# Kernel tuning notes

Hardware: AMD Instinct MI355X
Metric: run time of the kernel (lower is better)

The kernel has to match this reference:

```python
import jax, jax.numpy as jnp
import numpy as np

B, S, D = 32, 577, 768
H, Dh = 12, 64  # num_attention_heads, attention_head_size = pruned_dim // heads


def setup_inputs() -> dict:
    key = jax.random.key(0)
    ks = jax.random.split(key, 7)
    s = 1.0 / np.sqrt(D)
    return {
        "hidden_states": jax.random.normal(ks[0], (B, S, D), dtype=jnp.float32),
        "Wq": jax.random.normal(ks[1], (D, H * Dh), dtype=jnp.float32) * s,
        "bq": jnp.zeros((H * Dh,), dtype=jnp.float32),
        "Wk": jax.random.normal(ks[2], (D, H * Dh), dtype=jnp.float32) * s,
        "bk": jnp.zeros((H * Dh,), dtype=jnp.float32),
        "Wv": jax.random.normal(ks[3], (D, H * Dh), dtype=jnp.float32) * s,
        "bv": jnp.zeros((H * Dh,), dtype=jnp.float32),
    }


def reference(hidden_states, Wq, bq, Wk, bk, Wv, bv):
    def heads(x):  # [B,S,H*Dh] -> [B,H,S,Dh]
        return x.reshape(B, S, H, Dh).transpose(0, 2, 1, 3)

    q = heads(hidden_states @ Wq + bq)
    k = heads(hidden_states @ Wk + bk)
    v = heads(hidden_states @ Wv + bv)

    scale = 1.0 / np.sqrt(Dh)
    scores = jnp.einsum("bhqd,bhkd->bhqk", q, k) * scale  # [B,H,S,S]
    probs = jax.nn.softmax(scores, axis=-1)  # dropout p=0.0 -> identity
    ctx = jnp.einsum("bhqk,bhkd->bhqd", probs, v)  # [B,H,S,Dh]
    ctx = ctx.transpose(0, 2, 1, 3).reshape(B, S, H * Dh)
    return ctx
```

## Files before the change

kernel.cpp:

```cpp
#include <hip/hip_runtime.h>

#define NB 32
#define SEQ 577
#define SP 640
#define DM 768
#define NH 12
#define DH 64
#define NC 10

typedef __attribute__((ext_vector_type(8))) short bf16x8;
typedef __attribute__((ext_vector_type(4))) short bf16x4;
typedef __attribute__((ext_vector_type(4))) float f32x4;
typedef __attribute__((ext_vector_type(2))) unsigned int u32x2;
typedef __attribute__((ext_vector_type(4))) unsigned int u32x4;
typedef unsigned short u16;

__device__ __forceinline__ u16 f2bf(float f) {
  unsigned int u = __builtin_bit_cast(unsigned int, f);
  u += 0x7fffu + ((u >> 16) & 1u);
  return (u16)(u >> 16);
}

__device__ __forceinline__ unsigned int pack_bf2(float a, float b) {
  unsigned int ua = __builtin_bit_cast(unsigned int, a) + 0x8000u;
  unsigned int ub = __builtin_bit_cast(unsigned int, b) + 0x8000u;
  return __builtin_amdgcn_perm(ub, ua, 0x07060302u);
}

__device__ __forceinline__ void g2l16(const void* g, void* lds) {
  __builtin_amdgcn_global_load_lds(
      (const __attribute__((address_space(1))) void*)g,
      (__attribute__((address_space(3))) void*)lds, 16, 0, 0);
}

__global__ void cvt_x_kernel(const float* __restrict__ X, u16* __restrict__ Xb, int n4) {
  int i = blockIdx.x * 256 + threadIdx.x;
  if (i >= n4) return;
  f32x4 v = *reinterpret_cast<const f32x4*>(X + (size_t)i * 4);
  u32x2 p;
  p[0] = (unsigned)f2bf(v[0]) | ((unsigned)f2bf(v[1]) << 16);
  p[1] = (unsigned)f2bf(v[2]) | ((unsigned)f2bf(v[3]) << 16);
  *reinterpret_cast<u32x2*>(Xb + (size_t)i * 4) = p;
}

__global__ void cvt_w_kernel(const float* __restrict__ Wq, const float* __restrict__ Wk,
                             const float* __restrict__ Wv, u16* __restrict__ Wt) {
  int idx = blockIdx.x * 256 + threadIdx.x;
  int m = blockIdx.y;
  const float* W = (m == 0) ? Wq : (m == 1) ? Wk : Wv;
  int k = idx / DM, n = idx - k * DM;
  Wt[(size_t)m * DM * DM + (size_t)n * DM + k] = f2bf(W[idx]);
}

__global__ __launch_bounds__(512, 2)
void qkv_gemm_kernel(const u16* __restrict__ Xb, const u16* __restrict__ Wt,
                     const float* __restrict__ bq, const float* __restrict__ bk,
                     const float* __restrict__ bv,
                     u16* __restrict__ Qw, u16* __restrict__ Kw, u16* __restrict__ Vw) {
  __shared__ alignas(16) u16 As[2][32 * 512];
  __shared__ alignas(16) u16 Bs[2][32 * 512];

  const int tid = threadIdx.x;
  const int lane = tid & 63;
  const int wid = tid >> 6;
  const int wm = wid >> 2, wn = wid & 3;
  const int l15 = lane & 15, lq = lane >> 4;

  const int flat = (blockIdx.z * 3 + blockIdx.y) * 80 + blockIdx.x;
  const int xcd = flat & 7;
  const int j8 = flat >> 3;
  const int xi = j8 / 9;
  const int yz = j8 - xi * 9;
  const int mt = xi * 8 + xcd;
  const int nt = yz % 3;
  const int qkv = yz / 3;

  const u16* Wm = Wt + (size_t)qkv * DM * DM;
  const float* bias = (qkv == 0) ? bq : (qkv == 1) ? bk : bv;

  const u16* gA[4];
  const u16* gB[4];
#pragma unroll
  for (int s = 0; s < 4; ++s) {
    const int e = wid * 4 + s;
    const int ti = e >> 1, hh = e & 1;
    int r = mt * 256 + ti * 16 + l15;
    int br = r / SP;
    int tr = r - br * SP;
    if (tr >= SEQ) tr = SEQ - 1;
    gA[s] = Xb + (size_t)(br * SEQ + tr) * DM + hh * 32 + lq * 8;
    gB[s] = Wm + (size_t)(nt * 256 + ti * 16 + l15) * DM + hh * 32 + lq * 8;
  }

  f32x4 acc[8][4];
#pragma unroll
  for (int i = 0; i < 8; ++i)
#pragma unroll
    for (int j = 0; j < 4; ++j)
#pragma unroll
      for (int r = 0; r < 4; ++r) acc[i][j][r] = 0.0f;

  auto stageA = [&](int buf, int kt) {
#pragma unroll
    for (int s = 0; s < 4; ++s)
      g2l16(gA[s] + kt * 64, &As[buf][(wid * 4 + s) * 512]);
  };
  auto stageB = [&](int buf, int kt) {
#pragma unroll
    for (int s = 0; s < 4; ++s)
      g2l16(gB[s] + kt * 64, &Bs[buf][(wid * 4 + s) * 512]);
  };

  stageA(0, 0);
  stageB(0, 0);
  asm volatile("s_waitcnt vmcnt(0)" ::: "memory");
  __builtin_amdgcn_s_barrier();

  const int NKT = DM / 64;
  for (int kt = 0; kt < NKT; ++kt) {
    const int buf = kt & 1;
    const bool more = (kt + 1 < NKT);
    bf16x8 af[4][2], bfr[4][2];

#pragma unroll
    for (int i = 0; i < 4; ++i)
#pragma unroll
      for (int h = 0; h < 2; ++h)
        af[i][h] = *reinterpret_cast<const bf16x8*>(
            &As[buf][(((wm * 8 + i) * 2 + h) * 64 + lane) * 8]);
#pragma unroll
    for (int j = 0; j < 2; ++j)
#pragma unroll
      for (int h = 0; h < 2; ++h)
        bfr[j][h] = *reinterpret_cast<const bf16x8*>(
            &Bs[buf][(((wn * 4 + j) * 2 + h) * 64 + lane) * 8]);
    if (more) stageA(buf ^ 1, kt + 1);
    __builtin_amdgcn_s_barrier();
    __builtin_amdgcn_s_setprio(1);
#pragma unroll
    for (int i = 0; i < 4; ++i)
#pragma unroll
      for (int j = 0; j < 2; ++j)
#pragma unroll
        for (int h = 0; h < 2; ++h)
          acc[i][j] = __builtin_amdgcn_mfma_f32_16x16x32_bf16(af[i][h], bfr[j][h], acc[i][j], 0, 0, 0);
    __builtin_amdgcn_s_setprio(0);
    __builtin_amdgcn_s_barrier();

#pragma unroll
    for (int j = 2; j < 4; ++j)
#pragma unroll
      for (int h = 0; h < 2; ++h)
        bfr[j][h] = *reinterpret_cast<const bf16x8*>(
            &Bs[buf][(((wn * 4 + j) * 2 + h) * 64 + lane) * 8]);
    if (more) stageB(buf ^ 1, kt + 1);
    __builtin_amdgcn_s_barrier();
    __builtin_amdgcn_s_setprio(1);
#pragma unroll
    for (int i = 0; i < 4; ++i)
#pragma unroll
      for (int j = 2; j < 4; ++j)
#pragma unroll
        for (int h = 0; h < 2; ++h)
          acc[i][j] = __builtin_amdgcn_mfma_f32_16x16x32_bf16(af[i][h], bfr[j][h], acc[i][j], 0, 0, 0);
    __builtin_amdgcn_s_setprio(0);
    __builtin_amdgcn_s_barrier();

#pragma unroll
    for (int i = 0; i < 4; ++i)
#pragma unroll
      for (int h = 0; h < 2; ++h)
        af[i][h] = *reinterpret_cast<const bf16x8*>(
            &As[buf][(((wm * 8 + 4 + i) * 2 + h) * 64 + lane) * 8]);
    __builtin_amdgcn_s_barrier();
    __builtin_amdgcn_s_setprio(1);
#pragma unroll
    for (int i = 0; i < 4; ++i)
#pragma unroll
      for (int j = 2; j < 4; ++j)
#pragma unroll
        for (int h = 0; h < 2; ++h)
          acc[4 + i][j] = __builtin_amdgcn_mfma_f32_16x16x32_bf16(af[i][h], bfr[j][h], acc[4 + i][j], 0, 0, 0);
    __builtin_amdgcn_s_setprio(0);
    __builtin_amdgcn_s_barrier();

    __builtin_amdgcn_s_setprio(1);
#pragma unroll
    for (int i = 0; i < 4; ++i)
#pragma unroll
      for (int j = 0; j < 2; ++j)
#pragma unroll
        for (int h = 0; h < 2; ++h)
          acc[4 + i][j] = __builtin_amdgcn_mfma_f32_16x16x32_bf16(af[i][h], bfr[j][h], acc[4 + i][j], 0, 0, 0);
    __builtin_amdgcn_s_setprio(0);
    asm volatile("s_waitcnt vmcnt(0)" ::: "memory");
    __builtin_amdgcn_s_barrier();
  }

  const float sfold = 0.18033688011112042f;
#pragma unroll
  for (int j = 0; j < 4; ++j) {
    const int col = nt * 256 + wn * 64 + j * 16 + l15;
    const int h = col >> 6;
    const int d = col & 63;
    const float bb = bias[col];
#pragma unroll
    for (int i = 0; i < 8; ++i) {
      const int rg = mt * 256 + wm * 128 + i * 16 + lq * 4;
      const int br = rg / SP;
      const int tr = rg - br * SP;
      if (qkv == 2) {
        float v0 = acc[i][j][0] + bb, v1 = acc[i][j][1] + bb;
        float v2 = acc[i][j][2] + bb, v3 = acc[i][j][3] + bb;
        u32x2 p;
        p[0] = (unsigned)f2bf(v0) | ((unsigned)f2bf(v1) << 16);
        p[1] = (unsigned)f2bf(v2) | ((unsigned)f2bf(v3) << 16);
        size_t o = ((size_t)(br * NH + h) * DH + d) * SP + tr;
        *reinterpret_cast<u32x2*>(Vw + o) = p;
      } else {
        u16* dst = ((qkv == 0) ? Qw : Kw) + ((size_t)(br * NH + h) * SP + tr) * DH + d;
#pragma unroll
        for (int r = 0; r < 4; ++r) {
          float v = acc[i][j][r] + bb;
          if (qkv == 0) v *= sfold;
          dst[r * DH] = f2bf(v);
        }
      }
    }
  }
}

#if __has_builtin(__builtin_amdgcn_mfma_f32_16x16x16bf16_1k)
#define MFMA16(a, b, c) __builtin_amdgcn_mfma_f32_16x16x16bf16_1k(a, b, c, 0, 0, 0)
#define HAVE_MFMA16 1
#elif __has_builtin(__builtin_amdgcn_mfma_f32_16x16x16_bf16)
#define MFMA16(a, b, c) __builtin_amdgcn_mfma_f32_16x16x16_bf16(a, b, c, 0, 0, 0)
#define HAVE_MFMA16 1
#else
#define HAVE_MFMA16 0
#endif

__global__ __launch_bounds__(256)
void attn_kernel(const u16* __restrict__ Qw, const u16* __restrict__ Kw,
                 const u16* __restrict__ Vw, float* __restrict__ out) {
  __shared__ alignas(16) u16 Kc[2][8 * 64 * 8];
  __shared__ alignas(16) u16 Vc[2][16 * 64 * 4];

  const int tid = threadIdx.x;
  const int lane = tid & 63;
  const int wid = tid >> 6;
  const int l15 = lane & 15, lq = lane >> 4;

  const int flat = blockIdx.y * 5 + blockIdx.x;
  const int w = (flat & 7) * 240 + (flat >> 3);
  const int qx = w % 5;
  const int bh = w / 5;
  const int b = bh / NH;
  const int h = bh - b * NH;
  const int q0 = qx * 128 + wid * 32;

  const u16* Qb = Qw + (size_t)bh * SP * DH;
  const u16* Kb = Kw + (size_t)bh * SP * DH;
  const u16* Vb = Vw + (size_t)bh * DH * SP;

  bf16x8 qf[2][2];
#pragma unroll
  for (int qt = 0; qt < 2; ++qt)
#pragma unroll
    for (int hf = 0; hf < 2; ++hf)
      qf[qt][hf] = *reinterpret_cast<const bf16x8*>(
          &Qb[(q0 + qt * 16 + l15) * DH + hf * 32 + lq * 8]);

  const u16* gK = Kb + (size_t)(wid * 16 + l15) * DH + lq * 8;
  const u16* gV = Vb + (size_t)(wid * 16 + l15) * SP + lq * 4;

  float mrow[2] = {-__builtin_inff(), -__builtin_inff()};
  float lrow[2] = {0.0f, 0.0f};
  f32x4 acc[2][4];
#pragma unroll
  for (int qt = 0; qt < 2; ++qt)
#pragma unroll
    for (int dt = 0; dt < 4; ++dt)
#pragma unroll
      for (int r = 0; r < 4; ++r) acc[qt][dt][r] = 0.0f;

  g2l16(gK, &Kc[0][(wid * 2 + 0) * 512]);
  g2l16(gK + 32, &Kc[0][(wid * 2 + 1) * 512]);
  {
    u32x2 v[4];
#pragma unroll
    for (int t = 0; t < 4; ++t)
      v[t] = *reinterpret_cast<const u32x2*>(gV + t * 16);
#pragma unroll
    for (int t = 0; t < 4; ++t)
      *reinterpret_cast<u32x2*>(&Vc[0][((wid * 4 + t) * 64 + lane) * 4]) = v[t];
  }
  __syncthreads();

  for (int c = 0; c < NC; ++c) {
    const int cur = c & 1;
    const int c0 = c * 64;
    u32x2 vn[4];
    if (c + 1 < NC) {
      const u16* gKn = gK + (size_t)(c0 + 64) * DH;
      g2l16(gKn, &Kc[cur ^ 1][(wid * 2 + 0) * 512]);
      g2l16(gKn + 32, &Kc[cur ^ 1][(wid * 2 + 1) * 512]);
#pragma unroll
      for (int t = 0; t < 4; ++t)
        vn[t] = *reinterpret_cast<const u32x2*>(gV + (c0 + 64) + t * 16);
    }

    f32x4 s[2][4];
    __builtin_amdgcn_s_setprio(1);
#pragma unroll
    for (int t = 0; t < 4; ++t) {
      bf16x8 kf0 = *reinterpret_cast<const bf16x8*>(&Kc[cur][((t * 2 + 0) * 64 + lane) * 8]);
      bf16x8 kf1 = *reinterpret_cast<const bf16x8*>(&Kc[cur][((t * 2 + 1) * 64 + lane) * 8]);
#pragma unroll
      for (int qt = 0; qt < 2; ++qt) {
        f32x4 z;
#pragma unroll
        for (int r = 0; r < 4; ++r) z[r] = 0.0f;
        z = __builtin_amdgcn_mfma_f32_16x16x32_bf16(kf0, qf[qt][0], z, 0, 0, 0);
        z = __builtin_amdgcn_mfma_f32_16x16x32_bf16(kf1, qf[qt][1], z, 0, 0, 0);
        s[qt][t] = z;
      }
    }
    __builtin_amdgcn_s_setprio(0);
    if (c0 + 64 > SEQ) {
#pragma unroll
      for (int qt = 0; qt < 2; ++qt)
#pragma unroll
        for (int t = 0; t < 4; ++t)
#pragma unroll
          for (int r = 0; r < 4; ++r) {
            int key = c0 + t * 16 + lq * 4 + r;
            s[qt][t][r] = (key < SEQ) ? s[qt][t][r] : -__builtin_inff();
          }
    }
    float alpha[2];
    unsigned int pku[2][4][2];
#pragma unroll
    for (int qt = 0; qt < 2; ++qt) {
      float mx = s[qt][0][0];
#pragma unroll
      for (int t = 0; t < 4; ++t)
#pragma unroll
        for (int r = 0; r < 4; ++r) mx = fmaxf(mx, s[qt][t][r]);
      mx = fmaxf(mx, __shfl_xor(mx, 16));
      mx = fmaxf(mx, __shfl_xor(mx, 32));
      float mn = fmaxf(mrow[qt], mx);
      alpha[qt] = __builtin_amdgcn_exp2f(mrow[qt] - mn);
      mrow[qt] = mn;
      float sm = 0.0f;
#pragma unroll
      for (int t = 0; t < 4; ++t) {
        float p0 = __builtin_amdgcn_exp2f(s[qt][t][0] - mn);
        float p1 = __builtin_amdgcn_exp2f(s[qt][t][1] - mn);
        float p2 = __builtin_amdgcn_exp2f(s[qt][t][2] - mn);
        float p3 = __builtin_amdgcn_exp2f(s[qt][t][3] - mn);
        sm += (p0 + p1) + (p2 + p3);
        pku[qt][t][0] = pack_bf2(p0, p1);
        pku[qt][t][1] = pack_bf2(p2, p3);
      }
      sm += __shfl_xor(sm, 16);
      sm += __shfl_xor(sm, 32);
      lrow[qt] = lrow[qt] * alpha[qt] + sm;
    }

#if HAVE_MFMA16
    __builtin_amdgcn_s_setprio(1);
#pragma unroll
    for (int dt = 0; dt < 4; ++dt) {
      bf16x4 vf[4];
#pragma unroll
      for (int t = 0; t < 4; ++t)
        vf[t] = *reinterpret_cast<const bf16x4*>(&Vc[cur][((dt * 4 + t) * 64 + lane) * 4]);
#pragma unroll
      for (int qt = 0; qt < 2; ++qt) {
        f32x4 a = acc[qt][dt];
#pragma unroll
        for (int r = 0; r < 4; ++r) a[r] *= alpha[qt];
#pragma unroll
        for (int t = 0; t < 4; ++t) {
          bf16x4 pf = __builtin_bit_cast(bf16x4, u32x2{pku[qt][t][0], pku[qt][t][1]});
          a = MFMA16(vf[t], pf, a);
        }
        acc[qt][dt] = a;
      }
    }
    __builtin_amdgcn_s_setprio(0);
#else
#pragma unroll
    for (int qt = 0; qt < 2; ++qt) {
      unsigned int bfrag[2][4];
#pragma unroll
      for (int hh = 0; hh < 2; ++hh)
#pragma unroll
        for (int w2 = 0; w2 < 4; ++w2) {
          int srcl = l15 + 16 * (2 * (lq & 1) + (w2 >> 1));
          unsigned int lo = (unsigned int)__shfl((int)pku[qt][2 * hh][w2 & 1], srcl);
          unsigned int hi = (unsigned int)__shfl((int)pku[qt][2 * hh + 1][w2 & 1], srcl);
          bfrag[hh][w2] = (lq < 2) ? lo : hi;
        }
#pragma unroll
      for (int dt = 0; dt < 4; ++dt) {
        f32x4 a = acc[qt][dt];
#pragma unroll
        for (int r = 0; r < 4; ++r) a[r] *= alpha[qt];
#pragma unroll
        for (int hh = 0; hh < 2; ++hh) {
          u32x2 w0 = *reinterpret_cast<const u32x2*>(&Vc[cur][((dt * 4 + 2 * hh) * 64 + lane) * 4]);
          u32x2 w1 = *reinterpret_cast<const u32x2*>(&Vc[cur][((dt * 4 + 2 * hh + 1) * 64 + lane) * 4]);
          u32x4 vw = {w0[0], w0[1], w1[0], w1[1]};
          u32x4 pw = {bfrag[hh][0], bfrag[hh][1], bfrag[hh][2], bfrag[hh][3]};
          a = __builtin_amdgcn_mfma_f32_16x16x32_bf16(
              __builtin_bit_cast(bf16x8, vw), __builtin_bit_cast(bf16x8, pw), a, 0, 0, 0);
        }
        acc[qt][dt] = a;
      }
    }
#endif

    if (c + 1 < NC) {
#pragma unroll
      for (int t = 0; t < 4; ++t)
        *reinterpret_cast<u32x2*>(&Vc[cur ^ 1][((wid * 4 + t) * 64 + lane) * 4]) = vn[t];
    }
    __syncthreads();
  }

#pragma unroll
  for (int qt = 0; qt < 2; ++qt) {
    int q = q0 + qt * 16 + l15;
    if (q < SEQ) {
      float rl = 1.0f / lrow[qt];
      float* orow = out + ((size_t)b * SEQ + q) * DM + h * DH;
#pragma unroll
      for (int dt = 0; dt < 4; ++dt) {
        f32x4 v = acc[qt][dt];
#pragma unroll
        for (int r = 0; r < 4; ++r) v[r] *= rl;
        *reinterpret_cast<f32x4*>(&orow[dt * 16 + lq * 4]) = v;
      }
    }
  }
}

extern "C" void kernel_launch(void* const* d_in, const int* in_sizes, int n_in,
                              void* d_out, int out_size, void* d_ws, size_t ws_size,
                              hipStream_t stream) {
  (void)in_sizes; (void)n_in; (void)out_size; (void)ws_size;
  const float* X  = (const float*)d_in[0];
  const float* Wq = (const float*)d_in[1];
  const float* bq = (const float*)d_in[2];
  const float* Wk = (const float*)d_in[3];
  const float* bk = (const float*)d_in[4];
  const float* Wv = (const float*)d_in[5];
  const float* bv = (const float*)d_in[6];
  float* out = (float*)d_out;

  char* ws = (char*)d_ws;
  u16* Xb = (u16*)ws;
  u16* Wt = (u16*)(ws + 28366848);
  u16* Qw = (u16*)(ws + 28366848 + 3538944);
  u16* Kw = Qw + (size_t)NB * NH * SP * DH;
  u16* Vw = Kw + (size_t)NB * NH * SP * DH;

  cvt_x_kernel<<<dim3(13848), 256, 0, stream>>>(X, Xb, 3545088);
  cvt_w_kernel<<<dim3(2304, 3), 256, 0, stream>>>(Wq, Wk, Wv, Wt);
  qkv_gemm_kernel<<<dim3(80, 3, 3), 512, 0, stream>>>(Xb, Wt, bq, bk, bv, Qw, Kw, Vw);
  attn_kernel<<<dim3(5, NB * NH), 256, 0, stream>>>(Qw, Kw, Vw, out);
}
```

Before: 343.6 us.

## Deepen QKV GEMM pipeline to four K=32 LDS stages with partial vmcnt waits

The QKV projection GEMM moves from a double-buffered K=64 tile to a four-buffer ring of K=32 tiles. Loads are issued three tiles ahead, and the full vmcnt(0) drain each iteration becomes a partial wait, so global-to-LDS copies overlap more MFMA work. The inner loop now has two MFMA phases instead of four, which removes some barriers per K step but doubles the iteration count. The risks are more loop overhead and a wait-count schedule that must stay correct in the tail iterations.

```diff
diff --git a/kernel.cpp b/kernel.cpp
--- a/kernel.cpp
+++ b/kernel.cpp
@@ -57,8 +57,8 @@
                      const float* __restrict__ bq, const float* __restrict__ bk,
                      const float* __restrict__ bv,
                      u16* __restrict__ Qw, u16* __restrict__ Kw, u16* __restrict__ Vw) {
-  __shared__ alignas(16) u16 As[2][32 * 512];
-  __shared__ alignas(16) u16 Bs[2][32 * 512];
+  __shared__ alignas(16) u16 As[4][16 * 512];
+  __shared__ alignas(16) u16 Bs[4][16 * 512];
 
   const int tid = threadIdx.x;
   const int lane = tid & 63;
@@ -78,18 +78,17 @@
   const u16* Wm = Wt + (size_t)qkv * DM * DM;
   const float* bias = (qkv == 0) ? bq : (qkv == 1) ? bk : bv;
 
-  const u16* gA[4];
-  const u16* gB[4];
-#pragma unroll
-  for (int s = 0; s < 4; ++s) {
-    const int e = wid * 4 + s;
-    const int ti = e >> 1, hh = e & 1;
-    int r = mt * 256 + ti * 16 + l15;
+  const u16* gA[2];
+  const u16* gB[2];
+#pragma unroll
+  for (int s = 0; s < 2; ++s) {
+    const int e = wid * 2 + s;
+    int r = mt * 256 + e * 16 + l15;
     int br = r / SP;
     int tr = r - br * SP;
     if (tr >= SEQ) tr = SEQ - 1;
-    gA[s] = Xb + (size_t)(br * SEQ + tr) * DM + hh * 32 + lq * 8;
-    gB[s] = Wm + (size_t)(nt * 256 + ti * 16 + l15) * DM + hh * 32 + lq * 8;
+    gA[s] = Xb + (size_t)(br * SEQ + tr) * DM + lq * 8;
+    gB[s] = Wm + (size_t)(nt * 256 + e * 16 + l15) * DM + lq * 8;
   }
 
   f32x4 acc[8][4];
@@ -101,99 +100,63 @@
       for (int r = 0; r < 4; ++r) acc[i][j][r] = 0.0f;
 
   auto stageA = [&](int buf, int kt) {
-#pragma unroll
-    for (int s = 0; s < 4; ++s)
-      g2l16(gA[s] + kt * 64, &As[buf][(wid * 4 + s) * 512]);
+    g2l16(gA[0] + kt * 32, &As[buf][(wid * 2 + 0) * 512]);
+    g2l16(gA[1] + kt * 32, &As[buf][(wid * 2 + 1) * 512]);
   };
   auto stageB = [&](int buf, int kt) {
-#pragma unroll
-    for (int s = 0; s < 4; ++s)
-      g2l16(gB[s] + kt * 64, &Bs[buf][(wid * 4 + s) * 512]);
+    g2l16(gB[0] + kt * 32, &Bs[buf][(wid * 2 + 0) * 512]);
+    g2l16(gB[1] + kt * 32, &Bs[buf][(wid * 2 + 1) * 512]);
   };
 
-  stageA(0, 0);
-  stageB(0, 0);
-  asm volatile("s_waitcnt vmcnt(0)" ::: "memory");
+  stageA(0, 0); stageB(0, 0);
+  stageA(1, 1); stageB(1, 1);
+  stageA(2, 2); stageB(2, 2);
+  asm volatile("s_waitcnt vmcnt(8)" ::: "memory");
   __builtin_amdgcn_s_barrier();
 
-  const int NKT = DM / 64;
+  const int NKT = DM / 32;
   for (int kt = 0; kt < NKT; ++kt) {
-    const int buf = kt & 1;
-    const bool more = (kt + 1 < NKT);
-    bf16x8 af[4][2], bfr[4][2];
+    const int buf = kt & 3;
+    const int nbuf = (kt + 3) & 3;
+    const bool more = (kt + 3 < NKT);
+    bf16x8 a03[4], bf4[4], a47[4];
 
 #pragma unroll
     for (int i = 0; i < 4; ++i)
-#pragma unroll
-      for (int h = 0; h < 2; ++h)
-        af[i][h] = *reinterpret_cast<const bf16x8*>(
-            &As[buf][(((wm * 8 + i) * 2 + h) * 64 + lane) * 8]);
-#pragma unroll
-    for (int j = 0; j < 2; ++j)
-#pragma unroll
-      for (int h = 0; h < 2; ++h)
-        bfr[j][h] = *reinterpret_cast<const bf16x8*>(
-            &Bs[buf][(((wn * 4 + j) * 2 + h) * 64 + lane) * 8]);
-    if (more) stageA(buf ^ 1, kt + 1);
+      a03[i] = *reinterpret_cast<const bf16x8*>(&As[buf][((wm * 8 + i) * 64 + lane) * 8]);
+#pragma unroll
+    for (int j = 0; j < 4; ++j)
+      bf4[j] = *reinterpret_cast<const bf16x8*>(&Bs[buf][((wn * 4 + j) * 64 + lane) * 8]);
+    if (more) stageA(nbuf, kt + 3);
     __builtin_amdgcn_s_barrier();
     __builtin_amdgcn_s_setprio(1);
 #pragma unroll
     for (int i = 0; i < 4; ++i)
 #pragma unroll
-      for (int j = 0; j < 2; ++j)
-#pragma unroll
-        for (int h = 0; h < 2; ++h)
-          acc[i][j] = __builtin_amdgcn_mfma_f32_16x16x32_bf16(af[i][h], bfr[j][h], acc[i][j], 0, 0, 0);
+      for (int j = 0; j < 4; ++j)
+        acc[i][j] = __builtin_amdgcn_mfma_f32_16x16x32_bf16(a03[i], bf4[j], acc[i][j], 0, 0, 0);
     __builtin_amdgcn_s_setprio(0);
     __builtin_amdgcn_s_barrier();
 
 #pragma unroll
-    for (int j = 2; j < 4; ++j)
-#pragma unroll
-      for (int h = 0; h < 2; ++h)
-        bfr[j][h] = *reinterpret_cast<const bf16x8*>(
-            &Bs[buf][(((wn * 4 + j) * 2 + h) * 64 + lane) * 8]);
-    if (more) stageB(buf ^ 1, kt + 1);
+    for (int i = 0; i < 4; ++i)
+      a47[i] = *reinterpret_cast<const bf16x8*>(&As[buf][((wm * 8 + 4 + i) * 64 + lane) * 8]);
+    if (more) stageB(nbuf, kt + 3);
+    if (kt <= NKT - 4) {
+      asm volatile("s_waitcnt vmcnt(8)" ::: "memory");
+    } else if (kt == NKT - 3) {
+      asm volatile("s_waitcnt vmcnt(4)" ::: "memory");
+    } else if (kt == NKT - 2) {
+      asm volatile("s_waitcnt vmcnt(0)" ::: "memory");
+    }
     __builtin_amdgcn_s_barrier();
     __builtin_amdgcn_s_setprio(1);
 #pragma unroll
     for (int i = 0; i < 4; ++i)
 #pragma unroll
-      for (int j = 2; j < 4; ++j)
-#pragma unroll
-        for (int h = 0; h < 2; ++h)
-          acc[i][j] = __builtin_amdgcn_mfma_f32_16x16x32_bf16(af[i][h], bfr[j][h], acc[i][j], 0, 0, 0);
+      for (int j = 0; j < 4; ++j)
+        acc[4 + i][j] = __builtin_amdgcn_mfma_f32_16x16x32_bf16(a47[i], bf4[j], acc[4 + i][j], 0, 0, 0);
     __builtin_amdgcn_s_setprio(0);
-    __builtin_amdgcn_s_barrier();
-
-#pragma unroll
-    for (int i = 0; i < 4; ++i)
-#pragma unroll
-      for (int h = 0; h < 2; ++h)
-        af[i][h] = *reinterpret_cast<const bf16x8*>(
-            &As[buf][(((wm * 8 + 4 + i) * 2 + h) * 64 + lane) * 8]);
-    __builtin_amdgcn_s_barrier();
-    __builtin_amdgcn_s_setprio(1);
-#pragma unroll
-    for (int i = 0; i < 4; ++i)
-#pragma unroll
-      for (int j = 2; j < 4; ++j)
-#pragma unroll
-        for (int h = 0; h < 2; ++h)
-          acc[4 + i][j] = __builtin_amdgcn_mfma_f32_16x16x32_bf16(af[i][h], bfr[j][h], acc[4 + i][j], 0, 0, 0);
-    __builtin_amdgcn_s_setprio(0);
-    __builtin_amdgcn_s_barrier();
-
-    __builtin_amdgcn_s_setprio(1);
-#pragma unroll
-    for (int i = 0; i < 4; ++i)
-#pragma unroll
-      for (int j = 0; j < 2; ++j)
-#pragma unroll
-        for (int h = 0; h < 2; ++h)
-          acc[4 + i][j] = __builtin_amdgcn_mfma_f32_16x16x32_bf16(af[i][h], bfr[j][h], acc[4 + i][j], 0, 0, 0);
-    __builtin_amdgcn_s_setprio(0);
-    asm volatile("s_waitcnt vmcnt(0)" ::: "memory");
     __builtin_amdgcn_s_barrier();
   }
 
```

Measured after the change: 326.6 us. -4.9%, faster.
